# Kernel optimization log

Measured on AMD Instinct MI355X. Metric: run time of the kernel, lower is better.

Reference implementation:

```python
import jax, jax.numpy as jnp
import numpy as np

N_NODES = 50000
N_EDGES = 800000
NUM_GRAPHS = 256
H = 128          # h_dim
C = H + 1        # CGConv channels = 129
Z = 2 * C + 1    # concat(x_i, x_j, edge_attr) = 259
N_GRAPH_LAYERS = 5
N_FC = 3
OUT_DIM = 1


def setup_inputs() -> dict:
    key = jax.random.key(0)
    ks = jax.random.split(key, 12)
    atoms = jax.random.randint(ks[0], (N_NODES,), 0, 119)
    pos = jax.random.normal(ks[1], (N_NODES, 3), dtype=jnp.float32)
    edge_index = jax.random.randint(ks[2], (2, N_EDGES), 0, N_NODES)
    batch = jnp.sort(jax.random.randint(ks[3], (N_NODES,), 0, NUM_GRAPHS))
    s = 0.05
    emb = jax.random.normal(ks[4], (119, H), dtype=jnp.float32)
    Wf = jax.random.normal(ks[5], (N_GRAPH_LAYERS, Z, C), dtype=jnp.float32) * s
    bf = jnp.zeros((N_GRAPH_LAYERS, C), dtype=jnp.float32)
    Ws = jax.random.normal(ks[6], (N_GRAPH_LAYERS, Z, C), dtype=jnp.float32) * s
    bs = jnp.zeros((N_GRAPH_LAYERS, C), dtype=jnp.float32)
    Wfc = jax.random.normal(ks[7], (N_FC, C, C), dtype=jnp.float32) * s
    bfc = jnp.zeros((N_FC, C), dtype=jnp.float32)
    Wout = jax.random.normal(ks[8], (C, OUT_DIM), dtype=jnp.float32) * s
    bout = jnp.zeros((OUT_DIM,), dtype=jnp.float32)
    return {"atoms": atoms, "pos": pos, "edge_index": edge_index, "batch": batch,
            "emb": emb, "Wf": Wf, "bf": bf, "Ws": Ws, "bs": bs,
            "Wfc": Wfc, "bfc": bfc, "Wout": Wout, "bout": bout}


def reference(atoms, pos, edge_index, batch, emb, Wf, bf, Ws, bs, Wfc, bfc, Wout, bout):
    n = atoms.shape[0]
    src, dst = edge_index[0], edge_index[1]  # PyG: x_j = x[src], x_i = x[dst], aggregate at dst
    # edge_attr = ||pos[src] - pos[dst]||, shape [E, 1]
    edge_attr = jnp.linalg.norm(pos[src] - pos[dst], axis=-1, keepdims=True)
    # node features: atom embedding + z-coordinate -> [N, 129]
    x = jnp.concatenate([emb[atoms], pos[:, 2:3]], axis=-1)
    for l in range(Wf.shape[0]):
        z = jnp.concatenate([x[dst], x[src], edge_attr], axis=-1)  # [E, 259]
        m = jax.nn.sigmoid(z @ Wf[l] + bf[l]) * jax.nn.softplus(z @ Ws[l] + bs[l])
        x = x + jax.ops.segment_sum(m, dst, num_segments=n)  # CGConv: aggr='add' + residual
    # mean pooling per graph
    sums = jax.ops.segment_sum(x, batch, num_segments=NUM_GRAPHS)
    cnts = jax.ops.segment_sum(jnp.ones((n, 1), x.dtype), batch, num_segments=NUM_GRAPHS)
    g = sums / jnp.maximum(cnts, 1.0)
    for l in range(Wfc.shape[0]):
        g = g @ Wfc[l] + bfc[l]
    return g @ Wout + bout
```

## Files before the change

### kernel.cpp

```cpp
#include <hip/hip_runtime.h>
#include <math.h>

#define N_NODES 50000
#define N_EDGES 800000
#define NUM_GRAPHS 256
#define NPADROWS 50048
#define CAP 64
#define XS 132
#define SCLN -1.44269504088896f
#define SCLP 1.44269504088896f
#define C693 0.69314718056f
#define LROW 264

typedef __attribute__((ext_vector_type(8))) short short8;
typedef __attribute__((ext_vector_type(4))) float f32x4;
typedef __attribute__((ext_vector_type(2))) float f32x2;

__device__ __forceinline__ float fast_rcp(float x) {
#if __has_builtin(__builtin_amdgcn_rcpf)
  return __builtin_amdgcn_rcpf(x);
#else
  return 1.0f / x;
#endif
}
__device__ __forceinline__ float EX2(float x) {
#if __has_builtin(__builtin_amdgcn_exp2f)
  return __builtin_amdgcn_exp2f(x);
#else
  return exp2f(x);
#endif
}
__device__ __forceinline__ float LG2(float x) {
#if __has_builtin(__builtin_amdgcn_logf)
  return __builtin_amdgcn_logf(x);
#else
  return log2f(x);
#endif
}
__device__ __forceinline__ unsigned f2bf(float x) {
  unsigned u = __float_as_uint(x);
  return (u + 0x7fffu + ((u >> 16) & 1u)) >> 16;
}
__device__ __forceinline__ float u2f(unsigned u) { return __uint_as_float(u); }
__device__ __forceinline__ f32x2 mk2(float a, float b) {
  f32x2 r; r.x = a; r.y = b; return r;
}
__device__ __forceinline__ f32x2 unp(unsigned u) {
  return mk2(u2f(u << 16), u2f(u & 0xffff0000u));
}
__device__ __forceinline__ void edge_ch2(f32x2 gf, f32x2 gs, float cmul, f32x2& acc) {
  f32x2 den = mk2(EX2(gf.x), EX2(gf.y)) + 1.0f;
  f32x2 lg = mk2(LG2(1.0f + EX2(-fabsf(gs.x))), LG2(1.0f + EX2(-fabsf(gs.y))));
  f32x2 sp = lg + __builtin_elementwise_max(gs, (f32x2)0.0f);
  f32x2 rt = mk2(fast_rcp(den.x), fast_rcp(den.y)) * sp;
  acc = __builtin_elementwise_fma(rt, (f32x2)cmul, acc);
}

__global__ void init_x(const int* __restrict__ atoms, const float* __restrict__ pos,
                       const float* __restrict__ emb, float* __restrict__ xf,
                       unsigned* __restrict__ xbu, float4* __restrict__ pos4) {
  int n = blockIdx.x;
  int t = threadIdx.x;
  int a = atoms[n];
  float2 e = *(const float2*)(emb + (size_t)a * 128 + 2 * t);
  xf[(size_t)n * XS + 2 * t] = e.x;
  xf[(size_t)n * XS + 2 * t + 1] = e.y;
  xbu[(size_t)n * 64 + t] = f2bf(e.x) | (f2bf(e.y) << 16);
  if (t == 0) xf[(size_t)n * XS + 128] = pos[n * 3 + 2];
  if (t == 1) pos4[n] = make_float4(pos[3 * n], pos[3 * n + 1], pos[3 * n + 2], 0.f);
}

__global__ void prep_b(const float* __restrict__ Wf, const float* __restrict__ Ws,
                       uint4* __restrict__ Bp, float* __restrict__ W128) {
  int idx = blockIdx.x * 256 + threadIdx.x;
  if (idx < 5 * 4 * 9 * 4 * 64) {
    int lane = idx & 63;
    int t = idx >> 6;
    int ks = t & 3; t >>= 2;
    int ct = t % 9; t /= 9;
    int g = t & 3;
    int l = t >> 2;
    const float* W = (g >= 2) ? Ws : Wf;
    int col = ct * 16 + (lane & 15);
    int kb = ks * 32 + (lane >> 4) * 8;
    unsigned u[4];
#pragma unroll
    for (int p = 0; p < 4; ++p) {
      unsigned lo = 0, hi = 0;
      if (col < 129) {
        int k0 = kb + 2 * p, k1 = k0 + 1;
        int r0 = (g & 1) ? 129 + k0 : k0;
        int r1 = (g & 1) ? 129 + k1 : k1;
        lo = f2bf(W[(size_t)(l * 259 + r0) * 129 + col]);
        hi = f2bf(W[(size_t)(l * 259 + r1) * 129 + col]);
      }
      u[p] = lo | (hi << 16);
    }
    Bp[idx] = make_uint4(u[0], u[1], u[2], u[3]);
  } else {
    int j = idx - 5 * 4 * 9 * 4 * 64;
    if (j >= 5 * 4 * 129) return;
    int c = j % 129;
    int t = j / 129;
    int g = t & 3;
    int l = t >> 2;
    const float* W = (g >= 2) ? Ws : Wf;
    int row = (g & 1) ? 257 : 128;
    W128[(l * 4 + g) * 129 + c] = W[(size_t)(l * 259 + row) * 129 + c];
  }
}

__global__ void build_csr(const int* __restrict__ ei, const float4* __restrict__ pos4,
                          const int* __restrict__ batch, int* __restrict__ cnt,
                          int2* __restrict__ csr, int* __restrict__ goff) {
  int e = blockIdx.x * 256 + threadIdx.x;
  if (e <= N_NODES) {
    int b = (e < N_NODES) ? batch[e] : NUM_GRAPHS;
    int bp = (e > 0) ? batch[e - 1] : -1;
    for (int g = bp + 1; g <= b; ++g) goff[g] = e;
  }
  if (e >= N_EDGES) return;
  int s = ei[e];
  int d = ei[N_EDGES + e];
  float4 ps = pos4[s];
  float4 pd = pos4[d];
  float dx = ps.x - pd.x, dy = ps.y - pd.y, dz = ps.z - pd.z;
  float ea = sqrtf(dx * dx + dy * dy + dz * dz);
  int p = atomicAdd(&cnt[d], 1);
  if (p < CAP) csr[d * CAP + p] = make_int2(s, __float_as_int(ea));
}

__global__ __launch_bounds__(256) void gemm_mfma(
    const unsigned* __restrict__ xbu, const float* __restrict__ xf,
    const uint4* __restrict__ Bp, const float* __restrict__ W128,
    const float* __restrict__ bfL, const float* __restrict__ bsL,
    unsigned short* __restrict__ Pdh, unsigned short* __restrict__ Pfs,
    unsigned* __restrict__ Pd128c, unsigned* __restrict__ Pc128, int layer) {
  __shared__ short smA[32 * 136];
  __shared__ unsigned short ldsD[32 * LROW];
  __shared__ unsigned short ldsS[32 * LROW];
  int n0 = blockIdx.x * 32;
  int tid = threadIdx.x;
  for (int ch = tid; ch < 512; ch += 256) {
    int row = ch >> 4, cq = ch & 15;
    *(uint4*)(&smA[row * 136 + cq * 8]) =
        *(const uint4*)(xbu + (size_t)(n0 + row) * 64 + cq * 4);
  }
  __syncthreads();
  int g = tid >> 6;
  int l = tid & 63;
  int q = l >> 4, c16 = l & 15;
  const short8* Bp8 = (const short8*)Bp;
  int bbase = (layer * 4 + g) * 9 * 4;
  f32x4 acc[2][9];
#pragma unroll
  for (int rt = 0; rt < 2; ++rt)
#pragma unroll
    for (int ct = 0; ct < 9; ++ct) acc[rt][ct] = (f32x4){0.f, 0.f, 0.f, 0.f};
#pragma unroll
  for (int ks = 0; ks < 4; ++ks) {
    short8 a0 = *(const short8*)(&smA[c16 * 136 + (ks * 4 + q) * 8]);
    short8 a1 = *(const short8*)(&smA[(16 + c16) * 136 + (ks * 4 + q) * 8]);
#pragma unroll
    for (int ct = 0; ct < 9; ++ct) {
      short8 b = Bp8[(size_t)(bbase + ct * 4 + ks) * 64 + l];
      acc[0][ct] = __builtin_amdgcn_mfma_f32_16x16x32_bf16(a0, b, acc[0][ct], 0, 0, 0);
      acc[1][ct] = __builtin_amdgcn_mfma_f32_16x16x32_bf16(a1, b, acc[1][ct], 0, 0, 0);
    }
  }
  const float* W1g = W128 + (layer * 4 + g) * 129;
  float x128[2][4];
#pragma unroll
  for (int rt = 0; rt < 2; ++rt)
#pragma unroll
    for (int r = 0; r < 4; ++r)
      x128[rt][r] = xf[(size_t)(n0 + rt * 16 + q * 4 + r) * XS + 128];
  float scale = (g < 2) ? SCLN : SCLP;
  unsigned short* ldsO = (g & 1) ? ldsS : ldsD;
  int soff = (g >= 2) ? 2 : 0;
  unsigned short* c128p = (g & 1) ? (unsigned short*)Pc128 : (unsigned short*)Pd128c;
  int c128o = (g >= 2) ? 1 : 0;
#pragma unroll
  for (int ct = 0; ct < 9; ++ct) {
    int col = ct * 16 + c16;
    float w1 = (col <= 128) ? W1g[col] : 0.0f;
    float bias = 0.0f;
    if (g == 0 && col <= 128) bias = bfL[col];
    if (g == 2 && col <= 128) bias = bsL[col];
#pragma unroll
    for (int rt = 0; rt < 2; ++rt) {
#pragma unroll
      for (int r = 0; r < 4; ++r) {
        int rl = rt * 16 + q * 4 + r;
        float v = scale * (acc[rt][ct][r] + x128[rt][r] * w1 + bias);
        unsigned short bv = (unsigned short)f2bf(v);
        if (col < 128) {
          ldsO[rl * LROW + ((col >> 1) << 2) + soff + (col & 1)] = bv;
        } else if (col == 128) {
          c128p[2 * (size_t)(n0 + rl) + c128o] = bv;
        }
      }
    }
  }
  __syncthreads();
#pragma unroll
  for (int i = tid; i < 2048; i += 256) {
    int img = i >> 10;
    int c = i & 1023;
    int row = c >> 5, part = c & 31;
    const unsigned short* src = (img ? ldsS : ldsD) + row * LROW + part * 8;
    unsigned short* dst = (img ? Pfs : Pdh) + (size_t)(n0 + row) * 256 + part * 8;
    *(uint4*)dst = *(const uint4*)src;
  }
}

__global__ __launch_bounds__(256) void edge_agg(
    const unsigned short* __restrict__ Pdh, const unsigned short* __restrict__ Pfs,
    const unsigned* __restrict__ Pd128c, const unsigned* __restrict__ Pc128,
    float* __restrict__ xf, unsigned* __restrict__ xbu, const int* __restrict__ cnt,
    const int2* __restrict__ csr, const float* __restrict__ WfL,
    const float* __restrict__ WsL) {
  int lane = threadIdx.x & 63;
  int half = lane >> 5;
  int l5 = lane & 31;
  int n = blockIdx.x * 4 + (threadIdx.x >> 6);
  if (n >= N_NODES) return;
  int nu = __builtin_amdgcn_readfirstlane(n);
  const float* wfl = WfL + 258 * 129;
  const float* wsl = WsL + 258 * 129;
  uint4 pdv = *(const uint4*)(Pdh + (size_t)nu * 256 + 8 * l5);
  f32x2 bfa = unp(pdv.x), bsa = unp(pdv.y), bfb = unp(pdv.z), bsb = unp(pdv.w);
  float2 wfa0 = *(const float2*)(wfl + 4 * l5);
  float2 wfb0 = *(const float2*)(wfl + 4 * l5 + 2);
  float2 wsa0 = *(const float2*)(wsl + 4 * l5);
  float2 wsb0 = *(const float2*)(wsl + 4 * l5 + 2);
  f32x2 wfa = mk2(SCLN * wfa0.x, SCLN * wfa0.y), wfb = mk2(SCLN * wfb0.x, SCLN * wfb0.y);
  f32x2 wsa = mk2(SCLP * wsa0.x, SCLP * wsa0.y), wsb = mk2(SCLP * wsb0.x, SCLP * wsb0.y);
  unsigned pd1 = Pd128c[nu];
  float bfc8 = u2f(pd1 << 16), bsc8 = u2f(pd1 & 0xffff0000u);
  float wfc8 = SCLN * wfl[128], wsc8 = SCLP * wsl[128];
  int m = cnt[nu];
  if (m > CAP) m = CAP;
  const int4* cb4 = (const int4*)(csr + (size_t)nu * CAP);
  const uint4* Pfq = (const uint4*)Pfs;
  float maskC = half ? 0.0f : C693;
  f32x2 accA = (f32x2)0.0f, accB = (f32x2)0.0f;

#define GATHER(qq) Pfq[(size_t)(half ? qq.z : qq.x) * 32 + l5]
#define COMPUTE(qq, gg, CM)                                                    \
  {                                                                            \
    f32x2 ea_ = (f32x2)__int_as_float(half ? qq.w : qq.y);                     \
    edge_ch2(__builtin_elementwise_fma(ea_, wfa, bfa + unp(gg.x)),             \
             __builtin_elementwise_fma(ea_, wsa, bsa + unp(gg.y)), CM, accA);  \
    edge_ch2(__builtin_elementwise_fma(ea_, wfb, bfb + unp(gg.z)),             \
             __builtin_elementwise_fma(ea_, wsb, bsb + unp(gg.w)), CM, accB);  \
  }

  int Pf = m >> 1;
  int4 qc = make_int4(0, 0, 0, 0);
  uint4 gc = make_uint4(0, 0, 0, 0);
  if (Pf > 0) {
    qc = cb4[0];
    gc = GATHER(qc);
  }
  for (int p = 0; p < Pf; ++p) {
    int4 qn = qc;
    uint4 gn = gc;
    if (p + 1 < Pf) {
      qn = cb4[p + 1];
      gn = GATHER(qn);
    }
    COMPUTE(qc, gc, C693);
    qc = qn;
    gc = gn;
  }
  if (m & 1) {
    int4 qt = cb4[Pf];
    f32x2 ea_ = (f32x2)__int_as_float(qt.y);
    uint4 gt = Pfq[(size_t)qt.x * 32 + l5];
    edge_ch2(__builtin_elementwise_fma(ea_, wfa, bfa + unp(gt.x)),
             __builtin_elementwise_fma(ea_, wsa, bsa + unp(gt.y)), maskC, accA);
    edge_ch2(__builtin_elementwise_fma(ea_, wfb, bfb + unp(gt.z)),
             __builtin_elementwise_fma(ea_, wsb, bsb + unp(gt.w)), maskC, accB);
  }
#undef GATHER
#undef COMPUTE

  accA.x += __shfl_xor(accA.x, 32, 64);
  accA.y += __shfl_xor(accA.y, 32, 64);
  accB.x += __shfl_xor(accB.x, 32, 64);
  accB.y += __shfl_xor(accB.y, 32, 64);

  float v2 = 0.f;
  if (lane < m) {
    int2 se = csr[(size_t)nu * CAP + lane];
    float ea = __int_as_float(se.y);
    unsigned pc = Pc128[se.x];
    float f2 = u2f(pc << 16), s2 = u2f(pc & 0xffff0000u);
    float gf2 = fmaf(ea, wfc8, bfc8 + f2);
    float gs2 = fmaf(ea, wsc8, bsc8 + s2);
    float sp2 = LG2(1.0f + EX2(-fabsf(gs2))) + fmaxf(gs2, 0.0f);
    v2 = C693 * fast_rcp(1.0f + EX2(gf2)) * sp2;
  }
#pragma unroll
  for (int off = 32; off; off >>= 1) v2 += __shfl_down(v2, off, 64);

  size_t xo = (size_t)nu * XS;
  if (half == 0) {
    float4 xv = *(const float4*)(xf + xo + 4 * l5);
    float4 res = make_float4(xv.x + accA.x, xv.y + accA.y, xv.z + accB.x, xv.w + accB.y);
    *(float4*)(xf + xo + 4 * l5) = res;
    *(uint2*)(xbu + (size_t)nu * 64 + 2 * l5) =
        make_uint2(f2bf(res.x) | (f2bf(res.y) << 16), f2bf(res.z) | (f2bf(res.w) << 16));
  }
  if (lane == 0) xf[xo + 128] += v2;
}

__global__ void pool2(const float* __restrict__ xf, const int* __restrict__ goff,
                      float* __restrict__ gsum) {
  int gph = blockIdx.x >> 2;
  int q = blockIdx.x & 3;
  int t = threadIdx.x;
  if (t >= 129) return;
  int s = goff[gph], e = goff[gph + 1];
  int len = e - s;
  int chunk = (len + 3) >> 2;
  int a = s + q * chunk;
  int b = a + chunk; if (b > e) b = e;
  if (a >= b) return;
  float acc = 0.f;
  for (int n = a; n < b; ++n) acc += xf[(size_t)n * XS + t];
  atomicAdd(&gsum[gph * XS + t], acc);
}

__global__ void fcout(const float* __restrict__ gsum, const int* __restrict__ goff,
                      const float* __restrict__ Wfc, const float* __restrict__ bfc,
                      const float* __restrict__ Wout, const float* __restrict__ bout,
                      float* __restrict__ out) {
  __shared__ float buf[2][XS];
  __shared__ float red[3];
  int i = blockIdx.x;
  int t = threadIdx.x;
  int len = goff[i + 1] - goff[i];
  float inv = fast_rcp(fmaxf((float)len, 1.0f));
  if (t < 129) buf[0][t] = gsum[i * XS + t] * inv;
  __syncthreads();
  int cur = 0;
#pragma unroll
  for (int l = 0; l < 3; ++l) {
    float s = 0.f;
    if (t < 129) {
      s = bfc[l * 129 + t];
      const float* W = Wfc + (size_t)l * 129 * 129;
#pragma unroll 4
      for (int k = 0; k < 129; ++k) s += buf[cur][k] * W[k * 129 + t];
    }
    __syncthreads();
    if (t < 129) buf[1 - cur][t] = s;
    cur = 1 - cur;
    __syncthreads();
  }
  float p = (t < 129) ? buf[cur][t] * Wout[t] : 0.f;
#pragma unroll
  for (int off = 32; off; off >>= 1) p += __shfl_down(p, off, 64);
  if ((t & 63) == 0) red[t >> 6] = p;
  __syncthreads();
  if (t == 0) out[i] = red[0] + red[1] + red[2] + bout[0];
}

extern "C" void kernel_launch(void* const* d_in, const int* in_sizes, int n_in,
                              void* d_out, int out_size, void* d_ws, size_t ws_size,
                              hipStream_t stream) {
  const int* atoms = (const int*)d_in[0];
  const float* pos = (const float*)d_in[1];
  const int* ei = (const int*)d_in[2];
  const int* batch = (const int*)d_in[3];
  const float* emb = (const float*)d_in[4];
  const float* Wf = (const float*)d_in[5];
  const float* bfp = (const float*)d_in[6];
  const float* Ws = (const float*)d_in[7];
  const float* bsp = (const float*)d_in[8];
  const float* Wfc = (const float*)d_in[9];
  const float* bfc = (const float*)d_in[10];
  const float* Wout = (const float*)d_in[11];
  const float* bout = (const float*)d_in[12];
  float* outp = (float*)d_out;

  uint4* Bp = (uint4*)d_ws;
  float* xf = (float*)(Bp + 46080);
  unsigned* xbu = (unsigned*)(xf + (size_t)NPADROWS * XS);
  unsigned short* Pdh = (unsigned short*)(xbu + (size_t)NPADROWS * 64);
  unsigned short* Pfs = Pdh + (size_t)NPADROWS * 256;
  float4* pos4 = (float4*)(Pfs + (size_t)NPADROWS * 256);
  float* W128 = (float*)(pos4 + N_NODES);
  float* gsum = W128 + 2580;
  int* goff = (int*)(gsum + 256 * XS);
  int* cnt = goff + 260;
  int2* csr = (int2*)(cnt + N_NODES + 2);
  unsigned* Pd128c = (unsigned*)(csr + (size_t)N_NODES * CAP);
  unsigned* Pc128 = Pd128c + NPADROWS;

  hipMemsetAsync(cnt, 0, N_NODES * sizeof(int), stream);
  hipMemsetAsync(gsum, 0, 256 * XS * sizeof(float), stream);

  init_x<<<N_NODES, 64, 0, stream>>>(atoms, pos, emb, xf, xbu, pos4);
  prep_b<<<(5 * 4 * 9 * 4 * 64 + 5 * 4 * 129 + 255) / 256, 256, 0, stream>>>(Wf, Ws, Bp,
                                                                             W128);
  build_csr<<<(N_EDGES + 255) / 256, 256, 0, stream>>>(ei, pos4, batch, cnt, csr, goff);

  for (int l = 0; l < 5; ++l) {
    gemm_mfma<<<NPADROWS / 32, 256, 0, stream>>>(xbu, xf, Bp, W128, bfp + l * 129,
                                                 bsp + l * 129, Pdh, Pfs, Pd128c,
                                                 Pc128, l);
    edge_agg<<<(N_NODES + 3) / 4, 256, 0, stream>>>(Pdh, Pfs, Pd128c, Pc128, xf, xbu,
                                                    cnt, csr,
                                                    Wf + (size_t)l * 259 * 129,
                                                    Ws + (size_t)l * 259 * 129);
  }

  pool2<<<NUM_GRAPHS * 4, 192, 0, stream>>>(xf, goff, gsum);
  fcout<<<NUM_GRAPHS, 192, 0, stream>>>(gsum, goff, Wfc, bfc, Wout, bout, outp);
}
```

Baseline: 734.2 us.

## Drop fp32 node state, keep bf16 features plus fp32 extra channel

Removes the fp32 node-feature array and keeps node state only as packed bf16, with a separate fp32 array for channel 128. The residual update reads and writes only the bf16 copy, pooling reads bf16 and writes per-quarter partial sums instead of atomics, and the two memsets are folded into init_x. The GEMM epilogue reuses one LDS image in two phases to halve shared memory, and uses a cheaper round-half-up bf16 conversion. This cuts memory traffic and launches, but accumulating the residual in bf16 across five layers loses precision.

New measurement: 743.0 us. About the same (+1.2%).

```diff
diff --git a/kernel.cpp b/kernel.cpp
--- a/kernel.cpp
+++ b/kernel.cpp
@@ -6,7 +6,6 @@
 #define NUM_GRAPHS 256
 #define NPADROWS 50048
 #define CAP 64
-#define XS 132
 #define SCLN -1.44269504088896f
 #define SCLP 1.44269504088896f
 #define C693 0.69314718056f
@@ -41,6 +40,14 @@
   unsigned u = __float_as_uint(x);
   return (u + 0x7fffu + ((u >> 16) & 1u)) >> 16;
 }
+__device__ __forceinline__ unsigned short bfr(float v) {
+  return (unsigned short)((__float_as_uint(v) + 0x8000u) >> 16);
+}
+__device__ __forceinline__ unsigned pkbfr(float lo, float hi) {
+  unsigned a = (__float_as_uint(lo) + 0x8000u) >> 16;
+  unsigned b = (__float_as_uint(hi) + 0x8000u) & 0xffff0000u;
+  return a | b;
+}
 __device__ __forceinline__ float u2f(unsigned u) { return __uint_as_float(u); }
 __device__ __forceinline__ f32x2 mk2(float a, float b) {
   f32x2 r; r.x = a; r.y = b; return r;
@@ -57,17 +64,17 @@
 }
 
 __global__ void init_x(const int* __restrict__ atoms, const float* __restrict__ pos,
-                       const float* __restrict__ emb, float* __restrict__ xf,
-                       unsigned* __restrict__ xbu, float4* __restrict__ pos4) {
+                       const float* __restrict__ emb, float* __restrict__ x128c,
+                       unsigned* __restrict__ xbu, float4* __restrict__ pos4,
+                       int* __restrict__ cnt) {
   int n = blockIdx.x;
   int t = threadIdx.x;
   int a = atoms[n];
   float2 e = *(const float2*)(emb + (size_t)a * 128 + 2 * t);
-  xf[(size_t)n * XS + 2 * t] = e.x;
-  xf[(size_t)n * XS + 2 * t + 1] = e.y;
   xbu[(size_t)n * 64 + t] = f2bf(e.x) | (f2bf(e.y) << 16);
-  if (t == 0) xf[(size_t)n * XS + 128] = pos[n * 3 + 2];
+  if (t == 0) x128c[n] = pos[n * 3 + 2];
   if (t == 1) pos4[n] = make_float4(pos[3 * n], pos[3 * n + 1], pos[3 * n + 2], 0.f);
+  if (t == 2) cnt[n] = 0;
 }
 
 __global__ void prep_b(const float* __restrict__ Wf, const float* __restrict__ Ws,
@@ -131,14 +138,13 @@
 }
 
 __global__ __launch_bounds__(256) void gemm_mfma(
-    const unsigned* __restrict__ xbu, const float* __restrict__ xf,
+    const unsigned* __restrict__ xbu, const float* __restrict__ x128c,
     const uint4* __restrict__ Bp, const float* __restrict__ W128,
     const float* __restrict__ bfL, const float* __restrict__ bsL,
     unsigned short* __restrict__ Pdh, unsigned short* __restrict__ Pfs,
     unsigned* __restrict__ Pd128c, unsigned* __restrict__ Pc128, int layer) {
   __shared__ short smA[32 * 136];
-  __shared__ unsigned short ldsD[32 * LROW];
-  __shared__ unsigned short ldsS[32 * LROW];
+  __shared__ unsigned short img[32 * LROW];
   int n0 = blockIdx.x * 32;
   int tid = threadIdx.x;
   for (int ch = tid; ch < 512; ch += 256) {
@@ -174,50 +180,57 @@
   for (int rt = 0; rt < 2; ++rt)
 #pragma unroll
     for (int r = 0; r < 4; ++r)
-      x128[rt][r] = xf[(size_t)(n0 + rt * 16 + q * 4 + r) * XS + 128];
+      x128[rt][r] = x128c[n0 + rt * 16 + q * 4 + r];
   float scale = (g < 2) ? SCLN : SCLP;
-  unsigned short* ldsO = (g & 1) ? ldsS : ldsD;
   int soff = (g >= 2) ? 2 : 0;
   unsigned short* c128p = (g & 1) ? (unsigned short*)Pc128 : (unsigned short*)Pd128c;
   int c128o = (g >= 2) ? 1 : 0;
-#pragma unroll
-  for (int ct = 0; ct < 9; ++ct) {
-    int col = ct * 16 + c16;
-    float w1 = (col <= 128) ? W1g[col] : 0.0f;
-    float bias = 0.0f;
-    if (g == 0 && col <= 128) bias = bfL[col];
-    if (g == 2 && col <= 128) bias = bsL[col];
-#pragma unroll
-    for (int rt = 0; rt < 2; ++rt) {
-#pragma unroll
-      for (int r = 0; r < 4; ++r) {
-        int rl = rt * 16 + q * 4 + r;
-        float v = scale * (acc[rt][ct][r] + x128[rt][r] * w1 + bias);
-        unsigned short bv = (unsigned short)f2bf(v);
-        if (col < 128) {
-          ldsO[rl * LROW + ((col >> 1) << 2) + soff + (col & 1)] = bv;
-        } else if (col == 128) {
-          c128p[2 * (size_t)(n0 + rl) + c128o] = bv;
+
+  auto epi = [&]() {
+#pragma unroll
+    for (int ct = 0; ct < 9; ++ct) {
+      int col = ct * 16 + c16;
+      float w1 = (col <= 128) ? W1g[col] : 0.0f;
+      float bias = 0.0f;
+      if (g == 0 && col <= 128) bias = bfL[col];
+      if (g == 2 && col <= 128) bias = bsL[col];
+#pragma unroll
+      for (int rt = 0; rt < 2; ++rt) {
+#pragma unroll
+        for (int r = 0; r < 4; ++r) {
+          int rl = rt * 16 + q * 4 + r;
+          float v = scale * (acc[rt][ct][r] + x128[rt][r] * w1 + bias);
+          if (col < 128) {
+            img[rl * LROW + ((col >> 1) << 2) + soff + (col & 1)] = bfr(v);
+          } else if (col == 128) {
+            c128p[2 * (size_t)(n0 + rl) + c128o] = bfr(v);
+          }
         }
       }
     }
-  }
-  __syncthreads();
-#pragma unroll
-  for (int i = tid; i < 2048; i += 256) {
-    int img = i >> 10;
-    int c = i & 1023;
-    int row = c >> 5, part = c & 31;
-    const unsigned short* src = (img ? ldsS : ldsD) + row * LROW + part * 8;
-    unsigned short* dst = (img ? Pfs : Pdh) + (size_t)(n0 + row) * 256 + part * 8;
-    *(uint4*)dst = *(const uint4*)src;
+  };
+
+  if ((g & 1) == 0) epi();
+  __syncthreads();
+  for (int i = tid; i < 1024; i += 256) {
+    int row = i >> 5, part = i & 31;
+    *(uint4*)(Pdh + (size_t)(n0 + row) * 256 + part * 8) =
+        *(const uint4*)(img + row * LROW + part * 8);
+  }
+  __syncthreads();
+  if (g & 1) epi();
+  __syncthreads();
+  for (int i = tid; i < 1024; i += 256) {
+    int row = i >> 5, part = i & 31;
+    *(uint4*)(Pfs + (size_t)(n0 + row) * 256 + part * 8) =
+        *(const uint4*)(img + row * LROW + part * 8);
   }
 }
 
 __global__ __launch_bounds__(256) void edge_agg(
     const unsigned short* __restrict__ Pdh, const unsigned short* __restrict__ Pfs,
     const unsigned* __restrict__ Pd128c, const unsigned* __restrict__ Pc128,
-    float* __restrict__ xf, unsigned* __restrict__ xbu, const int* __restrict__ cnt,
+    unsigned* __restrict__ xbu, float* __restrict__ x128c, const int* __restrict__ cnt,
     const int2* __restrict__ csr, const float* __restrict__ WfL,
     const float* __restrict__ WsL) {
   int lane = threadIdx.x & 63;
@@ -305,19 +318,18 @@
 #pragma unroll
   for (int off = 32; off; off >>= 1) v2 += __shfl_down(v2, off, 64);
 
-  size_t xo = (size_t)nu * XS;
   if (half == 0) {
-    float4 xv = *(const float4*)(xf + xo + 4 * l5);
-    float4 res = make_float4(xv.x + accA.x, xv.y + accA.y, xv.z + accB.x, xv.w + accB.y);
-    *(float4*)(xf + xo + 4 * l5) = res;
+    uint2 xv = *(const uint2*)(xbu + (size_t)nu * 64 + 2 * l5);
+    f32x2 xa = unp(xv.x) + accA;
+    f32x2 xb = unp(xv.y) + accB;
     *(uint2*)(xbu + (size_t)nu * 64 + 2 * l5) =
-        make_uint2(f2bf(res.x) | (f2bf(res.y) << 16), f2bf(res.z) | (f2bf(res.w) << 16));
-  }
-  if (lane == 0) xf[xo + 128] += v2;
-}
-
-__global__ void pool2(const float* __restrict__ xf, const int* __restrict__ goff,
-                      float* __restrict__ gsum) {
+        make_uint2(pkbfr(xa.x, xa.y), pkbfr(xb.x, xb.y));
+  }
+  if (lane == 0) x128c[nu] += v2;
+}
+
+__global__ void pool2(const unsigned* __restrict__ xbu, const float* __restrict__ x128c,
+                      const int* __restrict__ goff, float* __restrict__ gpart) {
   int gph = blockIdx.x >> 2;
   int q = blockIdx.x & 3;
   int t = threadIdx.x;
@@ -327,23 +339,34 @@
   int chunk = (len + 3) >> 2;
   int a = s + q * chunk;
   int b = a + chunk; if (b > e) b = e;
-  if (a >= b) return;
   float acc = 0.f;
-  for (int n = a; n < b; ++n) acc += xf[(size_t)n * XS + t];
-  atomicAdd(&gsum[gph * XS + t], acc);
-}
-
-__global__ void fcout(const float* __restrict__ gsum, const int* __restrict__ goff,
+  if (t < 128) {
+    int w = t >> 1, hi = t & 1;
+    for (int n = a; n < b; ++n) {
+      unsigned u = xbu[(size_t)n * 64 + w];
+      acc += hi ? u2f(u & 0xffff0000u) : u2f(u << 16);
+    }
+  } else {
+    for (int n = a; n < b; ++n) acc += x128c[n];
+  }
+  gpart[(size_t)(gph * 4 + q) * 132 + t] = acc;
+}
+
+__global__ void fcout(const float* __restrict__ gpart, const int* __restrict__ goff,
                       const float* __restrict__ Wfc, const float* __restrict__ bfc,
                       const float* __restrict__ Wout, const float* __restrict__ bout,
                       float* __restrict__ out) {
-  __shared__ float buf[2][XS];
+  __shared__ float buf[2][132];
   __shared__ float red[3];
   int i = blockIdx.x;
   int t = threadIdx.x;
   int len = goff[i + 1] - goff[i];
   float inv = fast_rcp(fmaxf((float)len, 1.0f));
-  if (t < 129) buf[0][t] = gsum[i * XS + t] * inv;
+  if (t < 129) {
+    float v = gpart[(size_t)(i * 4 + 0) * 132 + t] + gpart[(size_t)(i * 4 + 1) * 132 + t] +
+              gpart[(size_t)(i * 4 + 2) * 132 + t] + gpart[(size_t)(i * 4 + 3) * 132 + t];
+    buf[0][t] = v * inv;
+  }
   __syncthreads();
   int cur = 0;
 #pragma unroll
@@ -387,37 +410,34 @@
   float* outp = (float*)d_out;
 
   uint4* Bp = (uint4*)d_ws;
-  float* xf = (float*)(Bp + 46080);
-  unsigned* xbu = (unsigned*)(xf + (size_t)NPADROWS * XS);
+  unsigned* xbu = (unsigned*)(Bp + 46080);
   unsigned short* Pdh = (unsigned short*)(xbu + (size_t)NPADROWS * 64);
   unsigned short* Pfs = Pdh + (size_t)NPADROWS * 256;
   float4* pos4 = (float4*)(Pfs + (size_t)NPADROWS * 256);
   float* W128 = (float*)(pos4 + N_NODES);
-  float* gsum = W128 + 2580;
-  int* goff = (int*)(gsum + 256 * XS);
+  float* x128c = W128 + 2580;
+  float* gpart = x128c + NPADROWS;
+  int* goff = (int*)(gpart + 256 * 4 * 132);
   int* cnt = goff + 260;
-  int2* csr = (int2*)(cnt + N_NODES + 2);
+  int2* csr = (int2*)(cnt + N_NODES + 4);
   unsigned* Pd128c = (unsigned*)(csr + (size_t)N_NODES * CAP);
   unsigned* Pc128 = Pd128c + NPADROWS;
 
-  hipMemsetAsync(cnt, 0, N_NODES * sizeof(int), stream);
-  hipMemsetAsync(gsum, 0, 256 * XS * sizeof(float), stream);
-
-  init_x<<<N_NODES, 64, 0, stream>>>(atoms, pos, emb, xf, xbu, pos4);
+  init_x<<<N_NODES, 64, 0, stream>>>(atoms, pos, emb, x128c, xbu, pos4, cnt);
   prep_b<<<(5 * 4 * 9 * 4 * 64 + 5 * 4 * 129 + 255) / 256, 256, 0, stream>>>(Wf, Ws, Bp,
                                                                              W128);
   build_csr<<<(N_EDGES + 255) / 256, 256, 0, stream>>>(ei, pos4, batch, cnt, csr, goff);
 
   for (int l = 0; l < 5; ++l) {
-    gemm_mfma<<<NPADROWS / 32, 256, 0, stream>>>(xbu, xf, Bp, W128, bfp + l * 129,
+    gemm_mfma<<<NPADROWS / 32, 256, 0, stream>>>(xbu, x128c, Bp, W128, bfp + l * 129,
                                                  bsp + l * 129, Pdh, Pfs, Pd128c,
                                                  Pc128, l);
-    edge_agg<<<(N_NODES + 3) / 4, 256, 0, stream>>>(Pdh, Pfs, Pd128c, Pc128, xf, xbu,
+    edge_agg<<<(N_NODES + 3) / 4, 256, 0, stream>>>(Pdh, Pfs, Pd128c, Pc128, xbu, x128c,
                                                     cnt, csr,
                                                     Wf + (size_t)l * 259 * 129,
                                                     Ws + (size_t)l * 259 * 129);
   }
 
-  pool2<<<NUM_GRAPHS * 4, 192, 0, stream>>>(xf, goff, gsum);
-  fcout<<<NUM_GRAPHS, 192, 0, stream>>>(gsum, goff, Wfc, bfc, Wout, bout, outp);
-}
+  pool2<<<NUM_GRAPHS * 4, 192, 0, stream>>>(xbu, x128c, goff, gpart);
+  fcout<<<NUM_GRAPHS, 192, 0, stream>>>(gpart, goff, Wfc, bfc, Wout, bout, outp);
+}
```
